# Optimization experiments

Hardware: AMD Instinct MI355X
Metric: run time of the kernel (lower is better)

## Reference

```python
import jax, jax.numpy as jnp
import numpy as np

B, L, D = 2, 8192, 768
F = 768          # features
ORDER = 2
MAX_LEN = 8192
POS_DIM = 8
INNER = F * (ORDER + 1)  # 2304


def sine_pos_embedding(seq_len, dim=POS_DIM, max_seq_len=MAX_LEN):
    # sine_lin: linearly spaced periods, wrap to negative offsets, include linear coord
    offset = jnp.arange(seq_len)
    offset = jnp.concatenate([offset, offset - seq_len])          # [2L]
    periods = jnp.linspace(4.0, float(max_seq_len), dim // 2)
    freqs = 2.0 * jnp.pi / periods
    phases = jnp.outer(offset, freqs)                              # [2L, dim/2]
    pos_emb = jnp.concatenate((jnp.cos(phases), jnp.sin(phases)), axis=-1)
    pos_emb = jnp.concatenate((offset[:, None] / max_seq_len, pos_emb), axis=-1)
    return pos_emb  # [2L, dim+1]


def fftconv(v, h, bias):
    # v: [B, L, F], h: [1, 2L, F], bias: [1, 1, F]
    seqlen = v.shape[-2]
    n = 2 * seqlen
    h_f = jnp.fft.rfft(h, n=n, axis=-2)
    v_f = jnp.fft.rfft(v, n=n, axis=-2)
    y_f = v_f * h_f / n
    y = jnp.fft.irfft(y_f, axis=-2, n=n, norm='forward')[:, :seqlen, :]
    return y + v * bias


def setup_inputs() -> dict:
    key = jax.random.key(0)
    ks = jax.random.split(key, 13)
    inp = {
        'u': jax.random.normal(ks[0], (B, L, D), jnp.float32),
        'filter_w1': jax.random.normal(ks[1], (POS_DIM + 1, 64), jnp.float32) * (1.0 / np.sqrt(POS_DIM + 1)),
        'filter_b1': jnp.zeros((64,), jnp.float32),
        'filter_w2': jax.random.normal(ks[2], (64, ORDER * F), jnp.float32) * (1.0 / np.sqrt(64)),
        'filter_b2': jnp.zeros((ORDER * F,), jnp.float32),
        'decay': jax.random.uniform(ks[3], (ORDER, F), jnp.float32, 0.5, 4.0),
        'bias': jax.random.normal(ks[4], (ORDER, 1, 1, F), jnp.float32),  # bias_init=1
        'in_proj_w': jax.random.normal(ks[5], (D, INNER), jnp.float32) * 0.02,
        'in_proj_b': jnp.zeros((INNER,), jnp.float32),
        'short_w': jax.random.normal(ks[6], (3, 1, INNER), jnp.float32) * 0.02,  # grouped conv, groups=INNER
        'short_b': jnp.zeros((INNER,), jnp.float32),
        'out_w': jax.random.normal(ks[7], (F, D), jnp.float32) * (1.0 / np.sqrt(F)),
        'out_b': jnp.zeros((D,), jnp.float32),
    }
    return inp


def reference(u, filter_w1, filter_b1, filter_w2, filter_b2, decay, bias,
              in_proj_w, in_proj_b, short_w, short_b, out_w, out_b):
    seq_len = u.shape[-2]
    # --- implicit filter generation from positional embedding ---
    t = sine_pos_embedding(seq_len)[None, :, :]                    # [1, 2L, 9]
    h = jnp.sin(t @ filter_w1 + filter_b1) @ filter_w2 + filter_b2 # [1, 2L, ORDER*F]
    h = h.reshape(1, 2 * seq_len, ORDER, F)
    # --- modulation: exponential decay over normalized position ---
    mod_t = jnp.linspace(0.0, 1.0, MAX_LEN)[:seq_len]
    mod_t = jnp.concatenate([mod_t, jnp.flip(mod_t)])[None, :, None, None]  # [1, 2L, 1, 1]
    h = h * jnp.exp(-mod_t * jnp.abs(decay)[None, None, :, :])
    h = jnp.transpose(h, (2, 0, 1, 3))                             # [ORDER, 1, 2L, F]
    # --- input projection ---
    u = u @ in_proj_w + in_proj_b                                  # [B, L, INNER]
    # --- grouped short conv (depthwise, k=3, SAME) ---
    u = jax.lax.conv_general_dilated(
        u, short_w, window_strides=(1,), padding='SAME',
        dimension_numbers=('NWC', 'WIO', 'NWC'),
        feature_group_count=INNER) + short_b
    # --- hyena recurrence: v <- gate(fftconv(v)) ---
    splits = jnp.split(u, ORDER + 1, axis=-1)
    v, x = splits[0], splits[1:]
    for o in range(ORDER):
        v = fftconv(v, h[o], bias[o])
        v = v * x[o]
    # --- output projection ---
    y = v @ out_w + out_b
    return y
```

## Files before the change

### kernel.cpp

```cpp
#include <hip/hip_runtime.h>
#include <hip/hip_bf16.h>
#include <math.h>

#define L_SEQ 8192
#define NFFT  16384
#define NPAD  16896
#define F_DIM 768
#define D_DIM 768
#define C_IN  2304
#define NORD  2
#define NT    512
#define TWO_PI 6.2831853071795864769f

typedef unsigned short u16;
typedef __attribute__((ext_vector_type(8))) short bf16x8;
typedef __attribute__((ext_vector_type(4))) float f32x4;
struct __align__(8) U16x4 { u16 x, y, z, w; };

__device__ __forceinline__ float bf2f(u16 v) {
  unsigned u = ((unsigned)v) << 16; float f; __builtin_memcpy(&f, &u, 4); return f;
}
__device__ __forceinline__ u16 f2bf(float f) {
  __hip_bfloat16 h = __float2bfloat16(f); u16 r; __builtin_memcpy(&r, &h, 2); return r;
}

__device__ __forceinline__ int PAD(int i) { return i + (i >> 5); }

__device__ __forceinline__ void rot3(float ang, float& c1, float& s1,
                                     float& c2, float& s2, float& c3, float& s3)
{
  __sincosf(ang, &s1, &c1);
  c2 = c1 * c1 - s1 * s1; s2 = 2.0f * c1 * s1;
  c3 = c1 * c2 - s1 * s2; s3 = c1 * s2 + s1 * c2;
}

__device__ __forceinline__ float conv3b(const u16* __restrict__ row, int t,
                                        float w0, float w1, float w2, float sb)
{
  float l = (t > 0)         ? bf2f(row[t - 1]) : 0.0f;
  float c = bf2f(row[t]);
  float r = (t < L_SEQ - 1) ? bf2f(row[t + 1]) : 0.0f;
  return w0 * l + w1 * c + w2 * r + sb;
}


__device__ __forceinline__ void s1_l2_store(float* zr, float* zi, int g,
    const float yr[4][4], const float yi4[4][4])
{
  const float stw2 = -TWO_PI / 4096.0f;
  float c1, s1, c2, s2, c3, s3;
  rot3(stw2 * (float)g, c1, s1, c2, s2, c3, s3);
  #pragma unroll
  for (int k = 0; k < 4; ++k) {
    float t0r = yr[k][0] + yr[k][2], t0i = yi4[k][0] + yi4[k][2];
    float t1r = yr[k][0] - yr[k][2], t1i = yi4[k][0] - yi4[k][2];
    float t2r = yr[k][1] + yr[k][3], t2i = yi4[k][1] + yi4[k][3];
    float t3r = yr[k][1] - yr[k][3], t3i = yi4[k][1] - yi4[k][3];
    float o0r = t0r + t2r, o0i = t0i + t2i;
    float o1r = t1r + t3i, o1i = t1i - t3r;
    float o2r = t0r - t2r, o2i = t0i - t2i;
    float o3r = t1r - t3i, o3i = t1i + t3r;
    const int i0 = g + (k << 12);
    zr[PAD(i0       )] = o0r;               zi[PAD(i0       )] = o0i;
    zr[PAD(i0 + 1024)] = o1r*c1 - o1i*s1;   zi[PAD(i0 + 1024)] = o1r*s1 + o1i*c1;
    zr[PAD(i0 + 2048)] = o2r*c2 - o2i*s2;   zi[PAD(i0 + 2048)] = o2r*s2 + o2i*c2;
    zr[PAD(i0 + 3072)] = o3r*c3 - o3i*s3;   zi[PAD(i0 + 3072)] = o3r*s3 + o3i*c3;
  }
}

__device__ __forceinline__ void s1_zero_hi(float* zr, float* zi, int g,
    const float xr[2][4], const float xi[2][4])
{
  const float stw1 = -TWO_PI / 16384.0f;
  float yr[4][4], yi4[4][4];
  #pragma unroll
  for (int m = 0; m < 4; ++m) {
    const float x0r = xr[0][m], x0i = xi[0][m];
    const float x1r = xr[1][m], x1i = xi[1][m];
    const float y0r = x0r + x1r, y0i = x0i + x1i;
    const float y1r = x0r + x1i, y1i = x0i - x1r;
    const float y2r = x0r - x1r, y2i = x0i - x1i;
    const float y3r = x0r - x1i, y3i = x0i + x1r;
    float c1, s1, c2, s2, c3, s3;
    rot3(stw1 * (float)(g + (m << 10)), c1, s1, c2, s2, c3, s3);
    yr[0][m] = y0r;               yi4[0][m] = y0i;
    yr[1][m] = y1r*c1 - y1i*s1;   yi4[1][m] = y1r*s1 + y1i*c1;
    yr[2][m] = y2r*c2 - y2i*s2;   yi4[2][m] = y2r*s2 + y2i*c2;
    yr[3][m] = y3r*c3 - y3i*s3;   yi4[3][m] = y3r*s3 + y3i*c3;
  }
  s1_l2_store(zr, zi, g, yr, yi4);
}

__device__ __forceinline__ void fwd_mid_pairs(float* zr, float* zi, int tid)
{
  #pragma unroll
  for (int lq = 8; lq >= 4; lq -= 4) {
    const int q  = 1 << lq;
    const int q4 = q >> 2;
    const float stw1 = -TWO_PI / (float)(q << 2);
    const float stw2 = -TWO_PI / (float)q;
    for (int g = tid; g < NFFT / 16; g += NT) {
      const int j    = g & (q4 - 1);
      const int base = ((g >> (lq - 2)) << (lq + 2)) + j;
      float xr[4][4], xi4[4][4];
      #pragma unroll
      for (int k = 0; k < 4; ++k)
        #pragma unroll
        for (int m = 0; m < 4; ++m) {
          const int idx = PAD(base + m * q4 + k * q);
          xr[k][m] = zr[idx]; xi4[k][m] = zi[idx];
        }
      #pragma unroll
      for (int m = 0; m < 4; ++m) {
        float t0r = xr[0][m] + xr[2][m], t0i = xi4[0][m] + xi4[2][m];
        float t1r = xr[0][m] - xr[2][m], t1i = xi4[0][m] - xi4[2][m];
        float t2r = xr[1][m] + xr[3][m], t2i = xi4[1][m] + xi4[3][m];
        float t3r = xr[1][m] - xr[3][m], t3i = xi4[1][m] - xi4[3][m];
        float y0r = t0r + t2r, y0i = t0i + t2i;
        float y1r = t1r + t3i, y1i = t1i - t3r;
        float y2r = t0r - t2r, y2i = t0i - t2i;
        float y3r = t1r - t3i, y3i = t1i + t3r;
        float c1, s1, c2, s2, c3, s3;
        rot3(stw1 * (float)(j + m * q4), c1, s1, c2, s2, c3, s3);
        xr[0][m] = y0r;                xi4[0][m] = y0i;
        xr[1][m] = y1r * c1 - y1i * s1; xi4[1][m] = y1r * s1 + y1i * c1;
        xr[2][m] = y2r * c2 - y2i * s2; xi4[2][m] = y2r * s2 + y2i * c2;
        xr[3][m] = y3r * c3 - y3i * s3; xi4[3][m] = y3r * s3 + y3i * c3;
      }
      float c1, s1, c2, s2, c3, s3;
      rot3(stw2 * (float)j, c1, s1, c2, s2, c3, s3);
      #pragma unroll
      for (int k = 0; k < 4; ++k) {
        float t0r = xr[k][0] + xr[k][2], t0i = xi4[k][0] + xi4[k][2];
        float t1r = xr[k][0] - xr[k][2], t1i = xi4[k][0] - xi4[k][2];
        float t2r = xr[k][1] + xr[k][3], t2i = xi4[k][1] + xi4[k][3];
        float t3r = xr[k][1] - xr[k][3], t3i = xi4[k][1] - xi4[k][3];
        float y0r = t0r + t2r, y0i = t0i + t2i;
        float y1r = t1r + t3i, y1i = t1i - t3r;
        float y2r = t0r - t2r, y2i = t0i - t2i;
        float y3r = t1r - t3i, y3i = t1i + t3r;
        const int i0 = base + k * q;
        zr[PAD(i0         )] = y0r;            zi[PAD(i0         )] = y0i;
        zr[PAD(i0 +     q4)] = y1r*c1 - y1i*s1; zi[PAD(i0 +     q4)] = y1r*s1 + y1i*c1;
        zr[PAD(i0 + 2 * q4)] = y2r*c2 - y2i*s2; zi[PAD(i0 + 2 * q4)] = y2r*s2 + y2i*c2;
        zr[PAD(i0 + 3 * q4)] = y3r*c3 - y3i*s3; zi[PAD(i0 + 3 * q4)] = y3r*s3 + y3i*c3;
      }
    }
    __syncthreads();
  }
}

__device__ __forceinline__ void fused_final_spec_head(float* zr, float* zi,
    const __hip_bfloat162* __restrict__ H, int tid)
{
  for (int b = tid; b < NFFT / 4; b += NT) {
    const int i0 = b << 2;
    const int p  = PAD(i0);
    const float a0r = zr[p],     a0i = zi[p];
    const float a1r = zr[p + 1], a1i = zi[p + 1];
    const float a2r = zr[p + 2], a2i = zi[p + 2];
    const float a3r = zr[p + 3], a3i = zi[p + 3];
    float t0r = a0r + a2r, t0i = a0i + a2i;
    float t1r = a0r - a2r, t1i = a0i - a2i;
    float t2r = a1r + a3r, t2i = a1i + a3i;
    float t3r = a1r - a3r, t3i = a1i - a3i;
    float y0r = t0r + t2r, y0i = t0i + t2i;
    float y1r = t1r + t3i, y1i = t1i - t3r;
    float y2r = t0r - t2r, y2i = t0i - t2i;
    float y3r = t1r - t3i, y3i = t1i + t3r;
    const float4 hq = *(const float4*)&H[i0];
    __hip_bfloat162 h0, h1, h2, h3;
    __builtin_memcpy(&h0, &hq.x, 4); __builtin_memcpy(&h1, &hq.y, 4);
    __builtin_memcpy(&h2, &hq.z, 4); __builtin_memcpy(&h3, &hq.w, 4);
    float hr, hi;
    hr = __bfloat162float(h0.x); hi = __bfloat162float(h0.y);
    const float u0r = y0r*hr - y0i*hi, u0i = y0r*hi + y0i*hr;
    hr = __bfloat162float(h1.x); hi = __bfloat162float(h1.y);
    const float u1r = y1r*hr - y1i*hi, u1i = y1r*hi + y1i*hr;
    hr = __bfloat162float(h2.x); hi = __bfloat162float(h2.y);
    const float u2r = y2r*hr - y2i*hi, u2i = y2r*hi + y2i*hr;
    hr = __bfloat162float(h3.x); hi = __bfloat162float(h3.y);
    const float u3r = y3r*hr - y3i*hi, u3i = y3r*hi + y3i*hr;
    const float e0r = u0r + u2r, e0i = u0i + u2i;
    const float e1r = u0r - u2r, e1i = u0i - u2i;
    const float f0r = u1r + u3r, f0i = u1i + u3i;
    const float f1r = u1r - u3r, f1i = u1i - u3i;
    zr[p]     = e0r + f0r; zi[p]     = e0i + f0i;
    zr[p + 1] = e1r - f1i; zi[p + 1] = e1i + f1r;
    zr[p + 2] = e0r - f0r; zi[p + 2] = e0i - f0i;
    zr[p + 3] = e1r + f1i; zi[p + 3] = e1i - f1r;
  }
  __syncthreads();
}

__device__ __forceinline__ void inv_mid_pairs(float* zr, float* zi, int tid)
{
  #pragma unroll
  for (int lq = 2; lq <= 6; lq += 4) {
    const int q = 1 << lq;
    const int Q = q << 2;
    const float stw1 = TWO_PI / (float)(q << 2);
    const float stw2 = TWO_PI / (float)(Q << 2);
    for (int g = tid; g < NFFT / 16; g += NT) {
      const int j    = g & (q - 1);
      const int base = ((g >> lq) << (lq + 4)) + j;
      float xr[4][4], xi4[4][4];
      #pragma unroll
      for (int k = 0; k < 4; ++k)
        #pragma unroll
        for (int m = 0; m < 4; ++m) {
          const int idx = PAD(base + m * q + k * Q);
          xr[k][m] = zr[idx]; xi4[k][m] = zi[idx];
        }
      {
        float c1, s1, c2, s2, c3, s3;
        rot3(stw1 * (float)j, c1, s1, c2, s2, c3, s3);
        #pragma unroll
        for (int k = 0; k < 4; ++k) {
          float u0r = xr[k][0], u0i = xi4[k][0];
          float u1r = xr[k][1]*c1 - xi4[k][1]*s1, u1i = xr[k][1]*s1 + xi4[k][1]*c1;
          float u2r = xr[k][2]*c2 - xi4[k][2]*s2, u2i = xr[k][2]*s2 + xi4[k][2]*c2;
          float u3r = xr[k][3]*c3 - xi4[k][3]*s3, u3i = xr[k][3]*s3 + xi4[k][3]*c3;
          float e0r = u0r + u2r, e0i = u0i + u2i;
          float e1r = u0r - u2r, e1i = u0i - u2i;
          float f0r = u1r + u3r, f0i = u1i + u3i;
          float f1r = u1r - u3r, f1i = u1i - u3i;
          xr[k][0] = e0r + f0r; xi4[k][0] = e0i + f0i;
          xr[k][1] = e1r - f1i; xi4[k][1] = e1i + f1r;
          xr[k][2] = e0r - f0r; xi4[k][2] = e0i - f0i;
          xr[k][3] = e1r + f1i; xi4[k][3] = e1i - f1r;
        }
      }
      #pragma unroll
      for (int m = 0; m < 4; ++m) {
        float c1, s1, c2, s2, c3, s3;
        rot3(stw2 * (float)(j + m * q), c1, s1, c2, s2, c3, s3);
        float u0r = xr[0][m], u0i = xi4[0][m];
        float u1r = xr[1][m]*c1 - xi4[1][m]*s1, u1i = xr[1][m]*s1 + xi4[1][m]*c1;
        float u2r = xr[2][m]*c2 - xi4[2][m]*s2, u2i = xr[2][m]*s2 + xi4[2][m]*c2;
        float u3r = xr[3][m]*c3 - xi4[3][m]*s3, u3i = xr[3][m]*s3 + xi4[3][m]*c3;
        float e0r = u0r + u2r, e0i = u0i + u2i;
        float e1r = u0r - u2r, e1i = u0i - u2i;
        float f0r = u1r + u3r, f0i = u1i + u3i;
        float f1r = u1r - u3r, f1i = u1i - u3i;
        const int i0 = base + m * q;
        zr[PAD(i0        )] = e0r + f0r; zi[PAD(i0        )] = e0i + f0i;
        zr[PAD(i0 +     Q)] = e1r - f1i; zi[PAD(i0 +     Q)] = e1i + f1r;
        zr[PAD(i0 + 2 * Q)] = e0r - f0r; zi[PAD(i0 + 2 * Q)] = e0i - f0i;
        zr[PAD(i0 + 3 * Q)] = e1r + f1i; zi[PAD(i0 + 3 * Q)] = e1i - f1r;
      }
    }
    __syncthreads();
  }
}

template<bool TO_GLOBAL>
__device__ __forceinline__ void inv_last_gate(float* zr, float* zi,
    const u16* __restrict__ gr0, const u16* __restrict__ gr1,
    float w0, float w1, float w2, float wb, u16* __restrict__ outv, int tid)
{
  const float stw1 = TWO_PI / 4096.0f;
  const float stw2 = TWO_PI / 16384.0f;
  for (int g = tid; g < 1024; g += NT) {
    float xr[4][4], xi4[4][4];
    #pragma unroll
    for (int k = 0; k < 4; ++k)
      #pragma unroll
      for (int m = 0; m < 4; ++m) {
        const int idx = PAD(g + (m << 10) + (k << 12));
        xr[k][m] = zr[idx]; xi4[k][m] = zi[idx];
      }
    {
      float c1, s1, c2, s2, c3, s3;
      rot3(stw1 * (float)g, c1, s1, c2, s2, c3, s3);
      #pragma unroll
      for (int k = 0; k < 4; ++k) {
        float u0r = xr[k][0], u0i = xi4[k][0];
        float u1r = xr[k][1]*c1 - xi4[k][1]*s1, u1i = xr[k][1]*s1 + xi4[k][1]*c1;
        float u2r = xr[k][2]*c2 - xi4[k][2]*s2, u2i = xr[k][2]*s2 + xi4[k][2]*c2;
        float u3r = xr[k][3]*c3 - xi4[k][3]*s3, u3i = xr[k][3]*s3 + xi4[k][3]*c3;
        float e0r = u0r + u2r, e0i = u0i + u2i;
        float e1r = u0r - u2r, e1i = u0i - u2i;
        float f0r = u1r + u3r, f0i = u1i + u3i;
        float f1r = u1r - u3r, f1i = u1i - u3i;
        xr[k][0] = e0r + f0r; xi4[k][0] = e0i + f0i;
        xr[k][1] = e1r - f1i; xi4[k][1] = e1i + f1r;
        xr[k][2] = e0r - f0r; xi4[k][2] = e0i - f0i;
        xr[k][3] = e1r + f1i; xi4[k][3] = e1i - f1r;
      }
    }
    #pragma unroll
    for (int m = 0; m < 4; ++m) {
      float c1, s1, c2, s2, c3, s3;
      rot3(stw2 * (float)(g + (m << 10)), c1, s1, c2, s2, c3, s3);
      float u0r = xr[0][m], u0i = xi4[0][m];
      float u1r = xr[1][m]*c1 - xi4[1][m]*s1, u1i = xr[1][m]*s1 + xi4[1][m]*c1;
      float u2r = xr[2][m]*c2 - xi4[2][m]*s2, u2i = xr[2][m]*s2 + xi4[2][m]*c2;
      float u3r = xr[3][m]*c3 - xi4[3][m]*s3, u3i = xr[3][m]*s3 + xi4[3][m]*c3;
      float e0r = u0r + u2r, e0i = u0i + u2i;
      float e1r = u0r - u2r, e1i = u0i - u2i;
      float f0r = u1r + u3r, f0i = u1i + u3i;
      float f1r = u1r - u3r, f1i = u1i - u3i;
      const int t0 = g + (m << 10);
      const int t1 = t0 + 4096;
      const float o0r = e0r + f0r, o0i = e0i + f0i;
      const float o1r = e1r - f1i, o1i = e1i + f1r;
      const float a0 = conv3b(gr0, t0, w0, w1, w2, wb);
      const float b0 = conv3b(gr1, t0, w0, w1, w2, wb);
      const float a1 = conv3b(gr0, t1, w0, w1, w2, wb);
      const float b1 = conv3b(gr1, t1, w0, w1, w2, wb);
      if (TO_GLOBAL) {
        outv[t0]         = f2bf(o0r * a0);
        outv[L_SEQ + t0] = f2bf(o0i * b0);
        outv[t1]         = f2bf(o1r * a1);
        outv[L_SEQ + t1] = f2bf(o1i * b1);
      } else {
        zr[PAD(t0)] = o0r * a0;  zi[PAD(t0)] = o0i * b0;
        zr[PAD(t1)] = o1r * a1;  zi[PAD(t1)] = o1i * b1;
      }
    }
  }
  if (!TO_GLOBAL) __syncthreads();
}

__global__ __launch_bounds__(256)
void cast_bf16_kernel(const float* __restrict__ in, u16* __restrict__ out, int n4)
{
  int i = blockIdx.x * 256 + threadIdx.x;
  if (i < n4) {
    float4 v = ((const float4*)in)[i];
    U16x4 w; w.x = f2bf(v.x); w.y = f2bf(v.y); w.z = f2bf(v.z); w.w = f2bf(v.w);
    ((U16x4*)out)[i] = w;
  }
}

__global__ __launch_bounds__(256)
void transpose_cast_kernel(const float* __restrict__ in, u16* __restrict__ out,
                           int K, int N)
{
  __shared__ u16 tile[32][33];
  const int n0 = blockIdx.x * 32, k0 = blockIdx.y * 32;
  const int tx = threadIdx.x & 31, ty = threadIdx.x >> 5;
  #pragma unroll
  for (int i = 0; i < 32; i += 8)
    tile[ty + i][tx] = f2bf(in[(size_t)(k0 + ty + i) * N + n0 + tx]);
  __syncthreads();
  #pragma unroll
  for (int i = 0; i < 32; i += 8)
    out[(size_t)(n0 + ty + i) * K + k0 + tx] = tile[tx][ty + i];
}

__global__ __launch_bounds__(256)
void transpose_v_kernel(const u16* __restrict__ vb, u16* __restrict__ out)
{
  __shared__ u16 t2[64][65];
  const int m0 = blockIdx.x * 64, f0 = blockIdx.y * 64;
  const int tx = threadIdx.x & 63, ty = threadIdx.x >> 6;
  #pragma unroll
  for (int i = 0; i < 64; i += 4)
    t2[ty + i][tx] = vb[(size_t)(f0 + ty + i) * (2 * NFFT) + m0 + tx];
  __syncthreads();
  #pragma unroll
  for (int i = 0; i < 64; i += 4)
    out[(size_t)(m0 + ty + i) * F_DIM + f0 + tx] = t2[tx][ty + i];
}

__global__ __launch_bounds__(256)
void hid_gen_kernel(const float* __restrict__ w1, const float* __restrict__ b1,
                    u16* __restrict__ hidb)
{
  const int tid = threadIdx.x;
  const int r  = tid & 63;
  const int tb = tid >> 6;
  const float w1v0 = w1[r];
  const float b1v  = b1[r];
  float w1c[4], w1s[4];
  #pragma unroll
  for (int p = 0; p < 4; ++p) { w1c[p] = w1[(1 + p) * 64 + r]; w1s[p] = w1[(5 + p) * 64 + r]; }
  const int tau0 = blockIdx.x * 16;
  #pragma unroll
  for (int i = 0; i < 4; ++i) {
    const int tau = tau0 + tb + i * 4;
    const float off = (tau < L_SEQ) ? (float)tau : (float)(tau - NFFT);
    float acc = b1v + off * (1.0f / 8192.0f) * w1v0;
    #pragma unroll
    for (int p = 0; p < 4; ++p) {
      const double period = 4.0 + (8188.0 * p) / 3.0;
      const float freq = (float)(6.283185307179586476925287 / period);
      float sp, cp;
      sincosf(off * freq, &sp, &cp);
      acc += cp * w1c[p] + sp * w1s[p];
    }
    hidb[(size_t)tau * 64 + r] = f2bf(sinf(acc));
  }
}

template<int N_DIM, int K_DIM, int WMODE>
__global__ __launch_bounds__(256)
void mfma_gemm_kernel(const u16* __restrict__ A, const u16* __restrict__ B,
                      const float* __restrict__ bias, void* __restrict__ Cv,
                      const float* __restrict__ dk)
{
  constexpr int BK = 64;
  __shared__ u16 As[128 * BK];
  __shared__ u16 Bs[128 * BK];
  const int tid  = threadIdx.x;
  const int lane = tid & 63;
  const int wid  = tid >> 6;
  const int m0 = blockIdx.x * 128;
  const int n0 = blockIdx.y * 128;

  const u16* aPtr[4]; const u16* bPtr[4];
  #pragma unroll
  for (int i = 0; i < 4; ++i) {
    const int g = tid + (i << 8);
    aPtr[i] = A + (size_t)(m0 + (g >> 3)) * K_DIM + ((g & 7) << 3);
    bPtr[i] = B + (size_t)(n0 + (g >> 3)) * K_DIM + ((g & 7) << 3);
  }

  const int wm = (wid & 1) << 6;
  const int wn = (wid >> 1) << 6;
  int aoff[4], boff[4];
  #pragma unroll
  for (int f = 0; f < 4; ++f) {
    aoff[f] = (wm + f * 16 + (lane & 15)) * BK + ((lane >> 4) << 3);
    boff[f] = (wn + f * 16 + (lane & 15)) * BK + ((lane >> 4) << 3);
  }

  f32x4 acc[4][4];
  #pragma unroll
  for (int i = 0; i < 4; ++i)
    #pragma unroll
    for (int j = 0; j < 4; ++j)
      acc[i][j] = (f32x4){0.f, 0.f, 0.f, 0.f};

  for (int k0 = 0; k0 < K_DIM; k0 += BK) {
    #pragma unroll
    for (int i = 0; i < 4; ++i) {
      __builtin_amdgcn_global_load_lds(
          (const __attribute__((address_space(1))) void*)aPtr[i],
          (__attribute__((address_space(3))) void*)&As[(((wid << 6) + (i << 8)) << 3)],
          16, 0, 0);
      aPtr[i] += BK;
    }
    #pragma unroll
    for (int i = 0; i < 4; ++i) {
      __builtin_amdgcn_global_load_lds(
          (const __attribute__((address_space(1))) void*)bPtr[i],
          (__attribute__((address_space(3))) void*)&Bs[(((wid << 6) + (i << 8)) << 3)],
          16, 0, 0);
      bPtr[i] += BK;
    }
    __syncthreads();
    #pragma unroll
    for (int kk = 0; kk < 2; ++kk) {
      bf16x8 af[4], bg[4];
      #pragma unroll
      for (int f = 0; f < 4; ++f) af[f] = *(const bf16x8*)&As[aoff[f] + kk * 32];
      #pragma unroll
      for (int f = 0; f < 4; ++f) bg[f] = *(const bf16x8*)&Bs[boff[f] + kk * 32];
      #pragma unroll
      for (int fm = 0; fm < 4; ++fm)
        #pragma unroll
        for (int fn = 0; fn < 4; ++fn)
          acc[fm][fn] = __builtin_amdgcn_mfma_f32_16x16x32_bf16(
              af[fm], bg[fn], acc[fm][fn], 0, 0, 0);
    }
    __syncthreads();
  }

  if (WMODE == 0) {
    u16* C = (u16*)Cv;
    const int b = m0 >> 13;
    const int tbase = (m0 & (L_SEQ - 1)) + wm + ((lane >> 4) << 2);
    #pragma unroll
    for (int fn = 0; fn < 4; ++fn) {
      const int n = n0 + wn + fn * 16 + (lane & 15);
      const float bv = bias[n];
      u16* row = C + ((size_t)b * N_DIM + n) * L_SEQ;
      #pragma unroll
      for (int fm = 0; fm < 4; ++fm) {
        f32x4 v = acc[fm][fn];
        U16x4 w;
        w.x = f2bf(v[0] + bv); w.y = f2bf(v[1] + bv);
        w.z = f2bf(v[2] + bv); w.w = f2bf(v[3] + bv);
        *(U16x4*)&row[tbase + fm * 16] = w;
      }
    }
  } else if (WMODE == 1) {
    float* C = (float*)Cv;
    #pragma unroll
    for (int fn = 0; fn < 4; ++fn) {
      const int n = n0 + wn + fn * 16 + (lane & 15);
      const float bv = bias[n];
      #pragma unroll
      for (int fm = 0; fm < 4; ++fm) {
        const int mb = m0 + wm + fm * 16 + ((lane >> 4) << 2);
        f32x4 v = acc[fm][fn];
        #pragma unroll
        for (int r = 0; r < 4; ++r)
          C[(size_t)(mb + r) * N_DIM + n] = v[r] + bv;
      }
    }
  } else {
    u16* C = (u16*)Cv;
    #pragma unroll
    for (int fn = 0; fn < 4; ++fn) {
      const int n = n0 + wn + fn * 16 + (lane & 15);
      const float bv = bias[n];
      const float ad = fabsf(dk[n]);
      u16* row = C + (size_t)n * (2 * NFFT);
      #pragma unroll
      for (int fm = 0; fm < 4; ++fm) {
        const int mq = m0 + wm + fm * 16 + ((lane >> 4) << 2);
        f32x4 v = acc[fm][fn];
        U16x4 w;
        #pragma unroll
        for (int r = 0; r < 4; ++r) {
          const int t = mq + r;
          const float mt = (t < L_SEQ) ? (float)t * (1.0f / 8191.0f)
                                       : (float)(NFFT - 1 - t) * (1.0f / 8191.0f);
          const float dec = __expf(-mt * ad);
          ((u16*)&w)[r] = f2bf((v[r] + bv) * dec);
        }
        *(U16x4*)&row[mq] = w;
      }
    }
  }
}

__global__ __launch_bounds__(NT)
void filter_fft_kernel(float* __restrict__ hH, const float* __restrict__ bias)
{
  __shared__ float zr[NPAD];
  __shared__ float zi[NPAD];
  const int row = blockIdx.x;
  const int tid = threadIdx.x;
  float* h = hH + (size_t)row * NFFT;
  const u16* hb = (const u16*)h;

  const float stw1 = -TWO_PI / 16384.0f;
  for (int g = tid; g < 1024; g += NT) {
    float x[4][4];
    #pragma unroll
    for (int k = 0; k < 4; ++k)
      #pragma unroll
      for (int m = 0; m < 4; ++m)
        x[k][m] = bf2f(hb[g + (m << 10) + (k << 12)]);
    float yr[4][4], yi4[4][4];
    #pragma unroll
    for (int m = 0; m < 4; ++m) {
      const float t0 = x[0][m] + x[2][m];
      const float t1 = x[0][m] - x[2][m];
      const float t2 = x[1][m] + x[3][m];
      const float t3 = x[1][m] - x[3][m];
      float c1, s1, c2, s2, c3, s3;
      rot3(stw1 * (float)(g + (m << 10)), c1, s1, c2, s2, c3, s3);
      yr[0][m] = t0 + t2;           yi4[0][m] = 0.0f;
      yr[1][m] = t1*c1 + t3*s1;     yi4[1][m] = t1*s1 - t3*c1;
      yr[2][m] = (t0 - t2)*c2;      yi4[2][m] = (t0 - t2)*s2;
      yr[3][m] = t1*c3 - t3*s3;     yi4[3][m] = t1*s3 + t3*c3;
    }
    s1_l2_store(zr, zi, g, yr, yi4);
  }
  __syncthreads();
  fwd_mid_pairs(zr, zi, tid);

  const float bo = bias[row];
  const float s = 1.0f / (float)NFFT;
  __hip_bfloat162* out2 = (__hip_bfloat162*)h;
  for (int b = tid; b < NFFT / 4; b += NT) {
    const int i0 = b << 2;
    const int p  = PAD(i0);
    const float a0r = zr[p],     a0i = zi[p];
    const float a1r = zr[p + 1], a1i = zi[p + 1];
    const float a2r = zr[p + 2], a2i = zi[p + 2];
    const float a3r = zr[p + 3], a3i = zi[p + 3];
    const float t0r = a0r + a2r, t0i = a0i + a2i;
    const float t1r = a0r - a2r, t1i = a0i - a2i;
    const float t2r = a1r + a3r, t2i = a1i + a3i;
    const float t3r = a1r - a3r, t3i = a1i - a3i;
    union { float4 f4; __hip_bfloat162 hh[4]; } o;
    o.hh[0].x = __float2bfloat16((t0r + t2r + bo) * s);
    o.hh[0].y = __float2bfloat16((t0i + t2i) * s);
    o.hh[1].x = __float2bfloat16((t1r + t3i + bo) * s);
    o.hh[1].y = __float2bfloat16((t1i - t3r) * s);
    o.hh[2].x = __float2bfloat16((t0r - t2r + bo) * s);
    o.hh[2].y = __float2bfloat16((t0i - t2i) * s);
    o.hh[3].x = __float2bfloat16((t1r - t3i + bo) * s);
    o.hh[3].y = __float2bfloat16((t1i + t3r) * s);
    *(float4*)&out2[i0] = o.f4;
  }
}

__global__ __launch_bounds__(NT)
void fftconv_kernel(const u16* __restrict__ up, float* __restrict__ hH,
                    const float* __restrict__ sw, const float* __restrict__ sb)
{
  __shared__ float zr[NPAD];
  __shared__ float zi[NPAD];
  const int f = blockIdx.x;
  const int tid = threadIdx.x;
  float* rowf = hH + (size_t)f * NFFT;
  float* row1 = hH + (size_t)(F_DIM + f) * NFFT;

  const u16* u0 = up + (size_t)(0 * C_IN + f) * L_SEQ;
  const u16* u1 = up + (size_t)(1 * C_IN + f) * L_SEQ;
  const float vw0 = sw[f], vw1 = sw[C_IN + f], vw2 = sw[2 * C_IN + f];
  const float vb = sb[f];

  for (int g = tid; g < 1024; g += NT) {
    float xr[2][4], xi[2][4];
    #pragma unroll
    for (int k = 0; k < 2; ++k)
      #pragma unroll
      for (int m = 0; m < 4; ++m) {
        const int t = g + (m << 10) + (k << 12);
        xr[k][m] = conv3b(u0, t, vw0, vw1, vw2, vb);
        xi[k][m] = conv3b(u1, t, vw0, vw1, vw2, vb);
      }
    s1_zero_hi(zr, zi, g, xr, xi);
  }
  __syncthreads();
  fwd_mid_pairs(zr, zi, tid);
  fused_final_spec_head(zr, zi, (const __hip_bfloat162*)rowf, tid);
  inv_mid_pairs(zr, zi, tid);

  const int c0g = F_DIM + f;
  inv_last_gate<false>(zr, zi,
      up + (size_t)(0 * C_IN + c0g) * L_SEQ,
      up + (size_t)(1 * C_IN + c0g) * L_SEQ,
      sw[c0g], sw[C_IN + c0g], sw[2 * C_IN + c0g], sb[c0g], nullptr, tid);

  for (int g = tid; g < 1024; g += NT) {
    float xr[2][4], xi[2][4];
    #pragma unroll
    for (int k = 0; k < 2; ++k)
      #pragma unroll
      for (int m = 0; m < 4; ++m) {
        const int idx = PAD(g + (m << 10) + (k << 12));
        xr[k][m] = zr[idx]; xi[k][m] = zi[idx];
      }
    s1_zero_hi(zr, zi, g, xr, xi);
  }
  __syncthreads();
  fwd_mid_pairs(zr, zi, tid);
  fused_final_spec_head(zr, zi, (const __hip_bfloat162*)row1, tid);
  inv_mid_pairs(zr, zi, tid);

  const int c1g = 2 * F_DIM + f;
  inv_last_gate<true>(zr, zi,
      up + (size_t)(0 * C_IN + c1g) * L_SEQ,
      up + (size_t)(1 * C_IN + c1g) * L_SEQ,
      sw[c1g], sw[C_IN + c1g], sw[2 * C_IN + c1g], sb[c1g], (u16*)rowf, tid);
}

extern "C" void kernel_launch(void* const* d_in, const int* in_sizes, int n_in,
                              void* d_out, int out_size, void* d_ws, size_t ws_size,
                              hipStream_t stream)
{
  (void)in_sizes; (void)n_in; (void)out_size; (void)ws_size;
  const float* u     = (const float*)d_in[0];
  const float* fw1   = (const float*)d_in[1];
  const float* fb1   = (const float*)d_in[2];
  const float* fw2   = (const float*)d_in[3];
  const float* fb2   = (const float*)d_in[4];
  const float* decay = (const float*)d_in[5];
  const float* bias  = (const float*)d_in[6];
  const float* ipw   = (const float*)d_in[7];
  const float* ipb   = (const float*)d_in[8];
  const float* sw    = (const float*)d_in[9];
  const float* sb    = (const float*)d_in[10];
  const float* ow    = (const float*)d_in[11];
  const float* ob    = (const float*)d_in[12];
  float* out = (float*)d_out;

  char* ws = (char*)d_ws;
  u16*   up_t  = (u16*)(ws);
  float* hH    = (float*)(ws + 75497472);
  u16*   u_bf  = (u16*)(ws + 176160768);
  u16*   ipw_t = (u16*)(ws + 201326592);
  u16*   ow_t  = (u16*)(ws + 204865536);
  u16*   vt_t  = (u16*)(ws + 206045184);
  u16*   hidb  = (u16*)(ws);
  u16*   w2t   = (u16*)(ws + 2097152);

  cast_bf16_kernel<<<dim3(12288), 256, 0, stream>>>(u, u_bf, (2 * L_SEQ * D_DIM) / 4);
  transpose_cast_kernel<<<dim3(C_IN / 32, D_DIM / 32), 256, 0, stream>>>(ipw, ipw_t, D_DIM, C_IN);
  transpose_cast_kernel<<<dim3(D_DIM / 32, F_DIM / 32), 256, 0, stream>>>(ow, ow_t, F_DIM, D_DIM);

  hid_gen_kernel<<<dim3(NFFT / 16), 256, 0, stream>>>(fw1, fb1, hidb);
  transpose_cast_kernel<<<dim3(1536 / 32, 64 / 32), 256, 0, stream>>>(fw2, w2t, 64, 1536);
  mfma_gemm_kernel<1536, 64, 2><<<dim3(NFFT / 128, 1536 / 128), 256, 0, stream>>>(
      hidb, w2t, fb2, hH, decay);
  filter_fft_kernel<<<dim3(NORD * F_DIM), NT, 0, stream>>>(hH, bias);

  mfma_gemm_kernel<C_IN, D_DIM, 0><<<dim3(128, C_IN / 128), 256, 0, stream>>>(u_bf, ipw_t, ipb, up_t, nullptr);
  fftconv_kernel<<<dim3(F_DIM), NT, 0, stream>>>(up_t, hH, sw, sb);
  transpose_v_kernel<<<dim3(NFFT / 64, F_DIM / 64), 256, 0, stream>>>((const u16*)hH, vt_t);
  mfma_gemm_kernel<D_DIM, F_DIM, 1><<<dim3(128, D_DIM / 128), 256, 0, stream>>>(vt_t, ow_t, ob, out, nullptr);
}
```

Baseline: 508.1 us.

## Pack two real filter FFTs per complex FFT and fuse output transpose into GEMM

The filter FFT kernel now packs the two order filters for a feature into the real and imaginary parts of one complex 16384-point FFT. It uses a full radix-4 pass and separates the two spectra through conjugate symmetry with digit-reversed indexing, which halves the block count. The standalone transpose of the gated output is removed, and the output-projection GEMM gains a transposed-A path that reads the feature-major buffer directly and scatters it into LDS. The trade-off is a shared-memory scatter in the GEMM instead of the async global-to-LDS load, plus more FFT stages per filter block.

```diff
diff --git a/kernel.cpp b/kernel.cpp
--- a/kernel.cpp
+++ b/kernel.cpp
@@ -25,6 +25,12 @@
 }
 
 __device__ __forceinline__ int PAD(int i) { return i + (i >> 5); }
+
+__device__ __forceinline__ int rev4_14(int p) {
+  return ((p & 0x0003) << 12) | ((p & 0x000C) << 8) | ((p & 0x0030) << 4)
+       | ( p & 0x00C0       ) | ((p & 0x0300) >> 4) | ((p & 0x0C00) >> 8)
+       | ((p & 0x3000) >> 12);
+}
 
 __device__ __forceinline__ void rot3(float ang, float& c1, float& s1,
                                      float& c2, float& s2, float& c3, float& s3)
@@ -91,10 +97,11 @@
   s1_l2_store(zr, zi, g, yr, yi4);
 }
 
-__device__ __forceinline__ void fwd_mid_pairs(float* zr, float* zi, int tid)
-{
-  #pragma unroll
-  for (int lq = 8; lq >= 4; lq -= 4) {
+template<int LQ0>
+__device__ __forceinline__ void fwd_pairs(float* zr, float* zi, int tid)
+{
+  #pragma unroll
+  for (int lq = LQ0; lq >= 4; lq -= 4) {
     const int q  = 1 << lq;
     const int q4 = q >> 2;
     const float stw1 = -TWO_PI / (float)(q << 2);
@@ -351,21 +358,6 @@
 }
 
 __global__ __launch_bounds__(256)
-void transpose_v_kernel(const u16* __restrict__ vb, u16* __restrict__ out)
-{
-  __shared__ u16 t2[64][65];
-  const int m0 = blockIdx.x * 64, f0 = blockIdx.y * 64;
-  const int tx = threadIdx.x & 63, ty = threadIdx.x >> 6;
-  #pragma unroll
-  for (int i = 0; i < 64; i += 4)
-    t2[ty + i][tx] = vb[(size_t)(f0 + ty + i) * (2 * NFFT) + m0 + tx];
-  __syncthreads();
-  #pragma unroll
-  for (int i = 0; i < 64; i += 4)
-    out[(size_t)(m0 + ty + i) * F_DIM + f0 + tx] = t2[tx][ty + i];
-}
-
-__global__ __launch_bounds__(256)
 void hid_gen_kernel(const float* __restrict__ w1, const float* __restrict__ b1,
                     u16* __restrict__ hidb)
 {
@@ -395,7 +387,7 @@
   }
 }
 
-template<int N_DIM, int K_DIM, int WMODE>
+template<int N_DIM, int K_DIM, int WMODE, int ATRANS = 0, int ASTR = 0>
 __global__ __launch_bounds__(256)
 void mfma_gemm_kernel(const u16* __restrict__ A, const u16* __restrict__ B,
                       const float* __restrict__ bias, void* __restrict__ Cv,
@@ -414,7 +406,8 @@
   #pragma unroll
   for (int i = 0; i < 4; ++i) {
     const int g = tid + (i << 8);
-    aPtr[i] = A + (size_t)(m0 + (g >> 3)) * K_DIM + ((g & 7) << 3);
+    if (ATRANS == 0)
+      aPtr[i] = A + (size_t)(m0 + (g >> 3)) * K_DIM + ((g & 7) << 3);
     bPtr[i] = B + (size_t)(n0 + (g >> 3)) * K_DIM + ((g & 7) << 3);
   }
 
@@ -435,13 +428,27 @@
       acc[i][j] = (f32x4){0.f, 0.f, 0.f, 0.f};
 
   for (int k0 = 0; k0 < K_DIM; k0 += BK) {
-    #pragma unroll
-    for (int i = 0; i < 4; ++i) {
-      __builtin_amdgcn_global_load_lds(
-          (const __attribute__((address_space(1))) void*)aPtr[i],
-          (__attribute__((address_space(3))) void*)&As[(((wid << 6) + (i << 8)) << 3)],
-          16, 0, 0);
-      aPtr[i] += BK;
+    if (ATRANS) {
+      #pragma unroll
+      for (int i = 0; i < 4; ++i) {
+        const int g    = tid + (i << 8);
+        const int krow = g & 63;
+        const int mc   = g >> 6;
+        const uint4 v = *(const uint4*)&A[(size_t)(k0 + krow) * ASTR + m0 + mc * 8];
+        u16 e[8]; __builtin_memcpy(e, &v, 16);
+        #pragma unroll
+        for (int q = 0; q < 8; ++q)
+          As[(mc * 8 + q) * BK + krow] = e[q];
+      }
+    } else {
+      #pragma unroll
+      for (int i = 0; i < 4; ++i) {
+        __builtin_amdgcn_global_load_lds(
+            (const __attribute__((address_space(1))) void*)aPtr[i],
+            (__attribute__((address_space(3))) void*)&As[(((wid << 6) + (i << 8)) << 3)],
+            16, 0, 0);
+        aPtr[i] += BK;
+      }
     }
     #pragma unroll
     for (int i = 0; i < 4; ++i) {
@@ -534,44 +541,21 @@
 {
   __shared__ float zr[NPAD];
   __shared__ float zi[NPAD];
-  const int row = blockIdx.x;
+  const int f = blockIdx.x;
   const int tid = threadIdx.x;
-  float* h = hH + (size_t)row * NFFT;
-  const u16* hb = (const u16*)h;
-
-  const float stw1 = -TWO_PI / 16384.0f;
-  for (int g = tid; g < 1024; g += NT) {
-    float x[4][4];
-    #pragma unroll
-    for (int k = 0; k < 4; ++k)
-      #pragma unroll
-      for (int m = 0; m < 4; ++m)
-        x[k][m] = bf2f(hb[g + (m << 10) + (k << 12)]);
-    float yr[4][4], yi4[4][4];
-    #pragma unroll
-    for (int m = 0; m < 4; ++m) {
-      const float t0 = x[0][m] + x[2][m];
-      const float t1 = x[0][m] - x[2][m];
-      const float t2 = x[1][m] + x[3][m];
-      const float t3 = x[1][m] - x[3][m];
-      float c1, s1, c2, s2, c3, s3;
-      rot3(stw1 * (float)(g + (m << 10)), c1, s1, c2, s2, c3, s3);
-      yr[0][m] = t0 + t2;           yi4[0][m] = 0.0f;
-      yr[1][m] = t1*c1 + t3*s1;     yi4[1][m] = t1*s1 - t3*c1;
-      yr[2][m] = (t0 - t2)*c2;      yi4[2][m] = (t0 - t2)*s2;
-      yr[3][m] = t1*c3 - t3*s3;     yi4[3][m] = t1*s3 + t3*c3;
-    }
-    s1_l2_store(zr, zi, g, yr, yi4);
+  float* row0 = hH + (size_t)f * NFFT;
+  float* row1 = hH + (size_t)(F_DIM + f) * NFFT;
+  const u16* h0 = (const u16*)row0;
+  const u16* h1 = (const u16*)row1;
+
+  for (int t = tid; t < NFFT; t += NT) {
+    zr[PAD(t)] = bf2f(h0[t]);
+    zi[PAD(t)] = bf2f(h1[t]);
   }
   __syncthreads();
-  fwd_mid_pairs(zr, zi, tid);
-
-  const float bo = bias[row];
-  const float s = 1.0f / (float)NFFT;
-  __hip_bfloat162* out2 = (__hip_bfloat162*)h;
+  fwd_pairs<12>(zr, zi, tid);
   for (int b = tid; b < NFFT / 4; b += NT) {
-    const int i0 = b << 2;
-    const int p  = PAD(i0);
+    const int p = PAD(b << 2);
     const float a0r = zr[p],     a0i = zi[p];
     const float a1r = zr[p + 1], a1i = zi[p + 1];
     const float a2r = zr[p + 2], a2i = zi[p + 2];
@@ -580,16 +564,28 @@
     const float t1r = a0r - a2r, t1i = a0i - a2i;
     const float t2r = a1r + a3r, t2i = a1i + a3i;
     const float t3r = a1r - a3r, t3i = a1i - a3i;
-    union { float4 f4; __hip_bfloat162 hh[4]; } o;
-    o.hh[0].x = __float2bfloat16((t0r + t2r + bo) * s);
-    o.hh[0].y = __float2bfloat16((t0i + t2i) * s);
-    o.hh[1].x = __float2bfloat16((t1r + t3i + bo) * s);
-    o.hh[1].y = __float2bfloat16((t1i - t3r) * s);
-    o.hh[2].x = __float2bfloat16((t0r - t2r + bo) * s);
-    o.hh[2].y = __float2bfloat16((t0i - t2i) * s);
-    o.hh[3].x = __float2bfloat16((t1r - t3i + bo) * s);
-    o.hh[3].y = __float2bfloat16((t1i + t3r) * s);
-    *(float4*)&out2[i0] = o.f4;
+    zr[p]     = t0r + t2r; zi[p]     = t0i + t2i;
+    zr[p + 1] = t1r + t3i; zi[p + 1] = t1i - t3r;
+    zr[p + 2] = t0r - t2r; zi[p + 2] = t0i - t2i;
+    zr[p + 3] = t1r - t3i; zi[p + 3] = t1i + t3r;
+  }
+  __syncthreads();
+  const float bo0 = bias[f];
+  const float bo1 = bias[F_DIM + f];
+  const float s = 1.0f / (float)NFFT;
+  __hip_bfloat162* o0 = (__hip_bfloat162*)row0;
+  __hip_bfloat162* o1 = (__hip_bfloat162*)row1;
+  for (int p = tid; p < NFFT; p += NT) {
+    const int k  = rev4_14(p);
+    const int pb = rev4_14((NFFT - k) & (NFFT - 1));
+    const float ar = zr[PAD(p)],  ai = zi[PAD(p)];
+    const float br = zr[PAD(pb)], bi = zi[PAD(pb)];
+    const float h0r = 0.5f * (ar + br), h0i = 0.5f * (ai - bi);
+    const float h1r = 0.5f * (ai + bi), h1i = 0.5f * (br - ar);
+    __hip_bfloat162 w0, w1;
+    w0.x = __float2bfloat16((h0r + bo0) * s); w0.y = __float2bfloat16(h0i * s);
+    w1.x = __float2bfloat16((h1r + bo1) * s); w1.y = __float2bfloat16(h1i * s);
+    o0[p] = w0; o1[p] = w1;
   }
 }
 
@@ -622,7 +618,7 @@
     s1_zero_hi(zr, zi, g, xr, xi);
   }
   __syncthreads();
-  fwd_mid_pairs(zr, zi, tid);
+  fwd_pairs<8>(zr, zi, tid);
   fused_final_spec_head(zr, zi, (const __hip_bfloat162*)rowf, tid);
   inv_mid_pairs(zr, zi, tid);
 
@@ -644,7 +640,7 @@
     s1_zero_hi(zr, zi, g, xr, xi);
   }
   __syncthreads();
-  fwd_mid_pairs(zr, zi, tid);
+  fwd_pairs<8>(zr, zi, tid);
   fused_final_spec_head(zr, zi, (const __hip_bfloat162*)row1, tid);
   inv_mid_pairs(zr, zi, tid);
 
@@ -681,7 +677,6 @@
   u16*   u_bf  = (u16*)(ws + 176160768);
   u16*   ipw_t = (u16*)(ws + 201326592);
   u16*   ow_t  = (u16*)(ws + 204865536);
-  u16*   vt_t  = (u16*)(ws + 206045184);
   u16*   hidb  = (u16*)(ws);
   u16*   w2t   = (u16*)(ws + 2097152);
 
@@ -693,10 +688,10 @@
   transpose_cast_kernel<<<dim3(1536 / 32, 64 / 32), 256, 0, stream>>>(fw2, w2t, 64, 1536);
   mfma_gemm_kernel<1536, 64, 2><<<dim3(NFFT / 128, 1536 / 128), 256, 0, stream>>>(
       hidb, w2t, fb2, hH, decay);
-  filter_fft_kernel<<<dim3(NORD * F_DIM), NT, 0, stream>>>(hH, bias);
+  filter_fft_kernel<<<dim3(F_DIM), NT, 0, stream>>>(hH, bias);
 
   mfma_gemm_kernel<C_IN, D_DIM, 0><<<dim3(128, C_IN / 128), 256, 0, stream>>>(u_bf, ipw_t, ipb, up_t, nullptr);
   fftconv_kernel<<<dim3(F_DIM), NT, 0, stream>>>(up_t, hH, sw, sb);
-  transpose_v_kernel<<<dim3(NFFT / 64, F_DIM / 64), 256, 0, stream>>>((const u16*)hH, vt_t);
-  mfma_gemm_kernel<D_DIM, F_DIM, 1><<<dim3(128, D_DIM / 128), 256, 0, stream>>>(vt_t, ow_t, ob, out, nullptr);
-}
+  mfma_gemm_kernel<D_DIM, F_DIM, 1, 1, 2 * NFFT><<<dim3(128, D_DIM / 128), 256, 0, stream>>>(
+      (const u16*)hH, ow_t, ob, out, nullptr);
+}
```

Result: no change. 511.5 us (+0.7%).
